# Kernel tuning notes

Measured on AMD Instinct MI355X. Metric: run time of the kernel, lower is better.

The kernel has to match this reference:

```python
import jax, jax.numpy as jnp
import numpy as np

STRIDES = (8, 16, 32, 64, 128)
SCORE_THRESH = 0.05
IOU_THRESH = 0.6
MAX_DET = 1000


def _flat(p):
    # [B,C,H,W] -> [B,H*W,C]
    B, C = p.shape[0], p.shape[1]
    return jnp.transpose(p, (0, 2, 3, 1)).reshape(B, -1, C)


def _coords(h, w, stride):
    # FCOS coords_fmap2orig: center of each stride cell, (x, y) order -> [h*w, 2]
    sx = (jnp.arange(w, dtype=jnp.float32) * stride + stride // 2)
    sy = (jnp.arange(h, dtype=jnp.float32) * stride + stride // 2)
    yy, xx = jnp.meshgrid(sy, sx, indexing='ij')
    return jnp.stack([xx.ravel(), yy.ravel()], axis=-1)


def _nms_keep(boxes, valid, thr):
    # boxes: [M,4] sorted by descending score; valid: [M] bool. Greedy NMS keep mask.
    x1, y1, x2, y2 = boxes[:, 0], boxes[:, 1], boxes[:, 2], boxes[:, 3]
    area = (x2 - x1 + 1.0) * (y2 - y1 + 1.0)
    xx1 = jnp.maximum(x1[:, None], x1[None, :])
    yy1 = jnp.maximum(y1[:, None], y1[None, :])
    xx2 = jnp.minimum(x2[:, None], x2[None, :])
    yy2 = jnp.minimum(y2[:, None], y2[None, :])
    inter = jnp.clip(xx2 - xx1, 0.0) * jnp.clip(yy2 - yy1, 0.0)
    iou = inter / (area[:, None] + area[None, :] - inter)
    M = boxes.shape[0]
    idx = jnp.arange(M)

    def body(i, keep):
        sup = (idx > i) & (iou[i] > thr) & keep[i]
        return keep & (~sup)

    return jax.lax.fori_loop(0, M, body, valid)


def setup_inputs() -> dict:
    key = jax.random.key(0)
    B, C = 16, 80
    sizes = [(128, 128), (64, 64), (32, 32), (16, 16), (8, 8)]
    ks = jax.random.split(key, 15)
    inp = {}
    for i, (h, w) in enumerate(sizes):
        lvl = i + 3
        inp[f'cls_p{lvl}'] = jax.random.normal(ks[3 * i], (B, C, h, w), jnp.float32)
        inp[f'cnt_p{lvl}'] = jax.random.normal(ks[3 * i + 1], (B, 1, h, w), jnp.float32)
        inp[f'reg_p{lvl}'] = jax.random.uniform(ks[3 * i + 2], (B, 4, h, w), jnp.float32) * 100.0
    return inp


def _detect(cls_levels, cnt_levels, reg_levels):
    cls_logits = jnp.concatenate([_flat(p) for p in cls_levels], axis=1)  # [B,N,80]
    cnt_logits = jnp.concatenate([_flat(p) for p in cnt_levels], axis=1)  # [B,N,1]
    reg_preds = jnp.concatenate([_flat(p) for p in reg_levels], axis=1)   # [B,N,4]
    coords = jnp.concatenate(
        [_coords(p.shape[2], p.shape[3], s) for p, s in zip(cls_levels, STRIDES)], axis=0)  # [N,2]

    cls_preds = jax.nn.sigmoid(cls_logits)
    cnt_preds = jax.nn.sigmoid(cnt_logits)[..., 0]                        # [B,N]
    cls_max = jnp.max(cls_preds, axis=-1)                                 # [B,N]
    cls_classes = jnp.argmax(cls_preds, axis=-1) + 1                      # [B,N] 1-based labels
    scores = jnp.sqrt(cls_max * cnt_preds)                                # add_centerness

    boxes = jnp.concatenate(
        [coords[None] - reg_preds[..., :2], coords[None] + reg_preds[..., 2:]], axis=-1)  # [B,N,4]

    M = min(MAX_DET, scores.shape[1])
    topv, topi = jax.lax.top_k(scores, M)                                 # sorted desc
    classes_k = jnp.take_along_axis(cls_classes, topi, axis=1)            # [B,M]
    boxes_k = jnp.take_along_axis(boxes, topi[..., None], axis=1)         # [B,M,4]
    valid = topv >= SCORE_THRESH

    def per_image(b, s, c, v):
        # class-aware NMS via coordinate offset trick
        off = c.astype(b.dtype) * (jnp.max(b) + 1.0)
        keep = _nms_keep(b + off[:, None], v, IOU_THRESH)
        kf = keep.astype(s.dtype)
        return s * kf, c * keep.astype(c.dtype), b * kf[:, None]

    return jax.vmap(per_image)(boxes_k, topv, classes_k, valid)


def reference(cls_p3, cnt_p3, reg_p3, cls_p4, cnt_p4, reg_p4, cls_p5, cnt_p5, reg_p5,
              cls_p6, cnt_p6, reg_p6, cls_p7, cnt_p7, reg_p7):
    cls_levels = [cls_p3, cls_p4, cls_p5, cls_p6, cls_p7]
    cnt_levels = [cnt_p3, cnt_p4, cnt_p5, cnt_p6, cnt_p7]
    reg_levels = [reg_p3, reg_p4, reg_p5, reg_p6, reg_p7]
    return _detect(cls_levels, cnt_levels, reg_levels)
```

## Files before the change

### kernel.cpp

```cpp
#include <hip/hip_runtime.h>
#include <math.h>

#define NB 16
#define NC 80
#define NA 21824
#define NM 1000
#define NHBINS 2048
#define CANDCAP 4096

#define OFF_KEYS     0ul
#define OFF_CLSV     2793472ul
#define OFF_TOPSCORE 4190208ul
#define OFF_TOPCLS   4254208ul
#define OFF_TOPBOX   4318208ul
#define OFF_MAXB     4574208ul
#define OFF_MASK     4574272ul

__device__ __forceinline__ float sigm(float x) { return 1.0f / (1.0f + expf(-x)); }

__global__ __launch_bounds__(256, 6) void k_score(
    const float* __restrict__ cls3, const float* __restrict__ cnt3,
    const float* __restrict__ cls4, const float* __restrict__ cnt4,
    const float* __restrict__ cls5, const float* __restrict__ cnt5,
    const float* __restrict__ cls6, const float* __restrict__ cnt6,
    const float* __restrict__ cls7, const float* __restrict__ cnt7,
    unsigned long long* __restrict__ keys,
    float* __restrict__ clsv)
{
    __shared__ float lm[4 * 64 * 4];
    __shared__ int   lam[4 * 64 * 4];
    __shared__ float cm[256];
    __shared__ int   cam[256];
    const int b = blockIdx.y;
    const int tid = threadIdx.x;
    const int a = tid & 63, s = tid >> 6;
    const int g4 = blockIdx.x * 64 + a;

    if (g4 < (NA >> 2)) {
        const int n = g4 << 2;
        const float* clsP; int off, logW;
        if      (n < 16384) { clsP = cls3; off = 0;     logW = 7; }
        else if (n < 20480) { clsP = cls4; off = 16384; logW = 6; }
        else if (n < 21504) { clsP = cls5; off = 20480; logW = 5; }
        else if (n < 21760) { clsP = cls6; off = 21504; logW = 4; }
        else                { clsP = cls7; off = 21760; logW = 3; }
        const int HW4 = 1 << (2 * logW - 2);
        const int l4 = (n - off) >> 2;
        const float4* cp = (const float4*)clsP + (size_t)b * NC * HW4 + l4;
        const int c0 = s * 20;
        float4 buf[4];
#pragma unroll
        for (int u = 0; u < 4; u++) buf[u] = cp[(size_t)(c0 + u) * HW4];
        float m[4] = { -3.402823466e+38f, -3.402823466e+38f, -3.402823466e+38f, -3.402823466e+38f };
        int am[4] = { c0, c0, c0, c0 };
#pragma unroll
        for (int u = 0; u < 20; u++) {
            float4 vv = buf[u & 3];
            if (u + 4 < 20) buf[u & 3] = cp[(size_t)(c0 + u + 4) * HW4];
            const int c = c0 + u;
            if (vv.x > m[0]) { m[0] = vv.x; am[0] = c; }
            if (vv.y > m[1]) { m[1] = vv.y; am[1] = c; }
            if (vv.z > m[2]) { m[2] = vv.z; am[2] = c; }
            if (vv.w > m[3]) { m[3] = vv.w; am[3] = c; }
        }
#pragma unroll
        for (int k = 0; k < 4; k++) { lm[tid * 4 + k] = m[k]; lam[tid * 4 + k] = am[k]; }
    }
    __syncthreads();
    if (tid < 64 && (blockIdx.x * 64 + tid) < (NA >> 2)) {
        float M[4]; int AM[4];
#pragma unroll
        for (int k = 0; k < 4; k++) { M[k] = lm[tid * 4 + k]; AM[k] = lam[tid * 4 + k]; }
        for (int s2 = 1; s2 < 4; s2++) {
#pragma unroll
            for (int k = 0; k < 4; k++) {
                float vv = lm[(s2 * 64 + tid) * 4 + k];
                if (vv > M[k]) { M[k] = vv; AM[k] = lam[(s2 * 64 + tid) * 4 + k]; }
            }
        }
#pragma unroll
        for (int k = 0; k < 4; k++) { cm[tid * 4 + k] = M[k]; cam[tid * 4 + k] = AM[k]; }
    }
    __syncthreads();
    const int n2 = blockIdx.x * 256 + tid;
    if (n2 < NA) {
        const float* cntP; int off, logW;
        if      (n2 < 16384) { cntP = cnt3; off = 0;     logW = 7; }
        else if (n2 < 20480) { cntP = cnt4; off = 16384; logW = 6; }
        else if (n2 < 21504) { cntP = cnt5; off = 20480; logW = 5; }
        else if (n2 < 21760) { cntP = cnt6; off = 21504; logW = 4; }
        else                 { cntP = cnt7; off = 21760; logW = 3; }
        const int HW = 1 << (2 * logW);
        const int local = n2 - off;
        float cn = cntP[(size_t)b * HW + local];
        float M = cm[tid]; int AM = cam[tid];
        float sc = sqrtf(sigm(M) * sigm(cn));
        unsigned long long key = ((unsigned long long)__float_as_uint(sc) << 32)
                               | (unsigned int)(~(unsigned int)n2);
        keys[(size_t)b * NA + n2] = key;
        clsv[(size_t)b * NA + n2] = (float)(AM + 1);
    }
}

__global__ __launch_bounds__(256) void k_mid(
    const unsigned long long* __restrict__ keys, const float* __restrict__ clsv,
    const float* __restrict__ reg3, const float* __restrict__ reg4, const float* __restrict__ reg5,
    const float* __restrict__ reg6, const float* __restrict__ reg7,
    float* __restrict__ topscore, float* __restrict__ topcls,
    float4* __restrict__ topbox, float* __restrict__ maxb)
{
    __shared__ unsigned int sh_hist[NHBINS];
    __shared__ unsigned int sh_cur[NHBINS];
    __shared__ unsigned int sh_off[NHBINS];
    __shared__ unsigned int sh_subh[NHBINS];
    __shared__ unsigned int sh_subo[NHBINS];
    __shared__ unsigned int sh_subc[NHBINS];
    __shared__ unsigned long long scand[CANDCAP];
    __shared__ unsigned long long scand2[CANDCAP];
    __shared__ int part1[256];
    __shared__ int part2[8];
    __shared__ int sBoundary;
    __shared__ float redmax[256];

    const int b = blockIdx.x;
    const int tid = threadIdx.x;
    const unsigned long long* kb = keys + (size_t)b * NA;
    const ulonglong2* k2 = (const ulonglong2*)kb;

    for (int i = tid; i < NHBINS; i += 256) {
        sh_hist[i] = 0u; sh_cur[i] = 0u; sh_subh[i] = 0u; sh_subc[i] = 0u;
    }
    __syncthreads();

    for (int i = tid; i < NA / 2; i += 256) {
        ulonglong2 v = k2[i];
        atomicAdd(&sh_hist[(unsigned int)(v.x >> 51)], 1u);
        atomicAdd(&sh_hist[(unsigned int)(v.y >> 51)], 1u);
    }
    __syncthreads();

    { int s = 0; for (int i = 0; i < 8; i++) s += (int)sh_hist[tid * 8 + i]; part1[tid] = s; }
    __syncthreads();
    if (tid < 8) { int s2 = 0; for (int t = 0; t < 32; t++) s2 += part1[tid * 32 + t]; part2[tid] = s2; }
    __syncthreads();

    if (tid == 0) {
        int acc = 0, sc;
        for (sc = 7; sc > 0; sc--) { if (acc + part2[sc] >= NM) break; acc += part2[sc]; }
        int t;
        for (t = sc * 32 + 31; t > sc * 32; t--) { if (acc + part1[t] >= NM) break; acc += part1[t]; }
        int bin;
        for (bin = t * 8 + 7; bin > t * 8; bin--) { if (acc + (int)sh_hist[bin] >= NM) break; acc += (int)sh_hist[bin]; }
        sBoundary = bin;
    }
    {
        const int g = tid >> 5;
        int acc = 0;
        for (int q = g + 1; q < 8; q++) acc += part2[q];
        for (int t2 = (g << 5) + 31; t2 > tid; t2--) acc += part1[t2];
        int run = acc;
        for (int k = 7; k >= 0; k--) { sh_off[tid * 8 + k] = (unsigned int)run; run += (int)sh_hist[tid * 8 + k]; }
    }
    __syncthreads();

    const unsigned int boundary = (unsigned int)sBoundary;
    int total = (int)(sh_off[boundary] + sh_hist[boundary]);
    int cnt = (total > CANDCAP) ? CANDCAP : total;
    const int s0 = (int)sh_off[boundary];
    const int Lb = cnt - s0;

    for (int i = tid; i < NA / 2; i += 256) {
        ulonglong2 v = k2[i];
        unsigned int b0 = (unsigned int)(v.x >> 51);
        if (b0 >= boundary) { unsigned int p = sh_off[b0] + atomicAdd(&sh_cur[b0], 1u); if (p < CANDCAP) scand[p] = v.x; }
        unsigned int b1 = (unsigned int)(v.y >> 51);
        if (b1 >= boundary) { unsigned int p = sh_off[b1] + atomicAdd(&sh_cur[b1], 1u); if (p < CANDCAP) scand[p] = v.y; }
    }
    __syncthreads();

    for (int k = tid; k < Lb; k += 256)
        atomicAdd(&sh_subh[(unsigned int)(scand[s0 + k] >> 40) & 2047u], 1u);
    __syncthreads();

    { int s = 0; for (int i = 0; i < 8; i++) s += (int)sh_subh[tid * 8 + i]; part1[tid] = s; }
    __syncthreads();
    if (tid < 8) { int s2 = 0; for (int t = 0; t < 32; t++) s2 += part1[tid * 32 + t]; part2[tid] = s2; }
    __syncthreads();
    {
        const int g = tid >> 5;
        int acc = 0;
        for (int q = g + 1; q < 8; q++) acc += part2[q];
        for (int t2 = (g << 5) + 31; t2 > tid; t2--) acc += part1[t2];
        int run = acc;
        for (int k = 7; k >= 0; k--) { sh_subo[tid * 8 + k] = (unsigned int)run; run += (int)sh_subh[tid * 8 + k]; }
    }
    __syncthreads();

    for (int k = tid; k < Lb; k += 256) {
        unsigned long long v = scand[s0 + k];
        unsigned int sb = (unsigned int)(v >> 40) & 2047u;
        unsigned int p = sh_subo[sb] + atomicAdd(&sh_subc[sb], 1u);
        scand2[p] = v;
    }
    __syncthreads();

    float mymax = -3.402823466e+38f;
    for (int idx = tid; idx < cnt; idx += 256) {
        const unsigned long long key = (idx < s0) ? scand[idx] : scand2[idx - s0];
        const unsigned int bin = (unsigned int)(key >> 51);
        int rank;
        if (bin > boundary) {
            int g0 = (int)sh_off[bin];
            int g1 = g0 + (int)sh_hist[bin];
            rank = g0;
            for (int j = g0; j < g1; j++) rank += (scand[j] > key);
        } else {
            unsigned int sb = (unsigned int)(key >> 40) & 2047u;
            int t0 = (int)sh_subo[sb];
            int t1 = t0 + (int)sh_subh[sb];
            rank = s0 + t0;
            for (int j = t0; j < t1; j++) rank += (scand2[j] > key);
        }
        if (rank < NM) {
            const unsigned int ai = ~(unsigned int)key;
            const float* regP; int lvloff, W, logW, st;
            if      (ai < 16384) { regP = reg3; lvloff = 0;     W = 128; logW = 7; st = 8;   }
            else if (ai < 20480) { regP = reg4; lvloff = 16384; W = 64;  logW = 6; st = 16;  }
            else if (ai < 21504) { regP = reg5; lvloff = 20480; W = 32;  logW = 5; st = 32;  }
            else if (ai < 21760) { regP = reg6; lvloff = 21504; W = 16;  logW = 4; st = 64;  }
            else                 { regP = reg7; lvloff = 21760; W = 8;   logW = 3; st = 128; }
            const int local = (int)ai - lvloff;
            const int HW = 1 << (2 * logW);
            const float* rp = regP + (size_t)b * 4 * HW + local;
            float r0 = rp[0], r1 = rp[HW], r2 = rp[2 * HW], r3 = rp[3 * HW];
            float cv = clsv[(size_t)b * NA + ai];
            const float hs = (float)(st >> 1);
            float cx = (float)((local & (W - 1)) * st) + hs;
            float cy = (float)((local >> logW) * st) + hs;
            float4 bxv = make_float4(cx - r0, cy - r1, cx + r2, cy + r3);
            topscore[b * NM + rank] = __uint_as_float((unsigned int)(key >> 32));
            topcls[b * NM + rank] = cv;
            topbox[b * NM + rank] = bxv;
            mymax = fmaxf(mymax, fmaxf(fmaxf(bxv.x, bxv.y), fmaxf(bxv.z, bxv.w)));
        }
    }
    redmax[tid] = mymax;
    __syncthreads();
    for (int sgap = 128; sgap > 0; sgap >>= 1) {
        if (tid < sgap) redmax[tid] = fmaxf(redmax[tid], redmax[tid + sgap]);
        __syncthreads();
    }
    if (tid == 0) maxb[b] = __fadd_rn(redmax[0], 1.0f);
}

__global__ __launch_bounds__(256) void k_iou(
    const float4* __restrict__ topbox, const float* __restrict__ topcls,
    const float* __restrict__ maxb, unsigned long long* __restrict__ maskArr)
{
    __shared__ float4 sB[NM];
    __shared__ float sA[NM];
    const int b = blockIdx.y;
    const int tid = threadIdx.x;
    const float mp1 = maxb[b];
    for (int r = tid; r < NM; r += 256) {
        float4 f = topbox[b * NM + r];
        float off = __fmul_rn(topcls[b * NM + r], mp1);
        f.x = __fadd_rn(f.x, off); f.y = __fadd_rn(f.y, off);
        f.z = __fadd_rn(f.z, off); f.w = __fadd_rn(f.w, off);
        sB[r] = f;
        sA[r] = __fmul_rn(__fadd_rn(__fsub_rn(f.z, f.x), 1.0f),
                          __fadd_rn(__fsub_rn(f.w, f.y), 1.0f));
    }
    __syncthreads();
    int task = blockIdx.x * 256 + tid;
    if (task >= NM * 16) return;
    int w = task / NM, i = task - w * NM;
    float4 bi = sB[i]; float ai = sA[i];
    unsigned long long bits = 0ULL;
    int j0 = w << 6;
    int jstart = (j0 > i + 1) ? j0 : i + 1;
    int jend = (j0 + 64 < NM) ? j0 + 64 : NM;
    for (int j = jstart; j < jend; j++) {
        float4 bj = sB[j];
        float xx1 = fmaxf(bi.x, bj.x);
        float yy1 = fmaxf(bi.y, bj.y);
        float xx2 = fminf(bi.z, bj.z);
        float yy2 = fminf(bi.w, bj.w);
        float iw = fmaxf(__fsub_rn(xx2, xx1), 0.0f);
        float ih = fmaxf(__fsub_rn(yy2, yy1), 0.0f);
        float inter = __fmul_rn(iw, ih);
        float denom = __fsub_rn(__fadd_rn(ai, sA[j]), inter);
        float iou = inter / denom;
        if (iou > 0.6f) bits |= (1ULL << (j - j0));
    }
    maskArr[((size_t)b * 16 + w) * NM + i] = bits;
}

__global__ __launch_bounds__(256) void k_nms_sweep(
    const unsigned long long* __restrict__ maskArr,
    const float* __restrict__ topscore, const float* __restrict__ topcls,
    const float4* __restrict__ topbox, float* __restrict__ out)
{
    __shared__ unsigned long long smask[16 * NM];
    __shared__ unsigned long long lremv[16];
    const int b = blockIdx.x;
    const int tid = threadIdx.x;
    const int j = tid & 63, q = tid >> 6;
    const unsigned long long* gmask = maskArr + (size_t)b * (16 * NM);

    {
        const ulonglong2* src = (const ulonglong2*)gmask;
        ulonglong2* dst = (ulonglong2*)smask;
        for (int idx = tid; idx < 8 * NM; idx += 256) dst[idx] = src[idx];
    }
    if (tid < 16) lremv[tid] = 0ULL;
    __syncthreads();
    for (int r = tid; r < NM; r += 256) {
        float s = topscore[b * NM + r];
        if (!(s >= 0.05f)) atomicOr(&lremv[r >> 6], 1ULL << (r & 63));
    }

    for (int w = 0; w < 16; w++) {
        __syncthreads();
        const int row = w * 64 + j;
        unsigned long long D = (row < NM) ? smask[w * NM + row] : 0ULL;
        unsigned int dlo = (unsigned int)D, dhi = (unsigned int)(D >> 32);
        unsigned long long sv = lremv[w];
        unsigned int slo = __builtin_amdgcn_readfirstlane((unsigned int)sv);
        unsigned int shi = __builtin_amdgcn_readfirstlane((unsigned int)(sv >> 32));
        unsigned long long s = ((unsigned long long)shi << 32) | slo;
#pragma unroll
        for (int bb = 0; bb < 64; bb++) {
            unsigned int rlo = __builtin_amdgcn_readlane(dlo, bb);
            unsigned int rhi = __builtin_amdgcn_readlane(dhi, bb);
            unsigned long long rowv = ((unsigned long long)rhi << 32) | rlo;
            unsigned long long t = s | rowv;
            s = ((s >> bb) & 1ULL) ? s : t;
        }
        if (tid == 0) lremv[w] = s;
        const unsigned long long kw = ~s;
        if ((kw >> j) & 1ULL) {
            for (int k = w + 1 + q; k < 16; k += 4) {
                unsigned long long v = (row < NM) ? smask[k * NM + row] : 0ULL;
                if (v) atomicOr(&lremv[k], v);
            }
        }
    }
    __syncthreads();

    for (int r = tid; r < NM; r += 256) {
        bool keep = !((lremv[r >> 6] >> (r & 63)) & 1ULL);
        float kf = keep ? 1.0f : 0.0f;
        out[b * NM + r] = topscore[b * NM + r] * kf;
        out[NB * NM + b * NM + r] = topcls[b * NM + r] * kf;
        float4 bx = topbox[b * NM + r];
        ((float4*)(out + 2 * NB * NM))[b * NM + r] = make_float4(bx.x * kf, bx.y * kf, bx.z * kf, bx.w * kf);
    }
}

extern "C" void kernel_launch(void* const* d_in, const int* in_sizes, int n_in,
                              void* d_out, int out_size, void* d_ws, size_t ws_size,
                              hipStream_t stream) {
    const float* cls3 = (const float*)d_in[0];
    const float* cnt3 = (const float*)d_in[1];
    const float* reg3 = (const float*)d_in[2];
    const float* cls4 = (const float*)d_in[3];
    const float* cnt4 = (const float*)d_in[4];
    const float* reg4 = (const float*)d_in[5];
    const float* cls5 = (const float*)d_in[6];
    const float* cnt5 = (const float*)d_in[7];
    const float* reg5 = (const float*)d_in[8];
    const float* cls6 = (const float*)d_in[9];
    const float* cnt6 = (const float*)d_in[10];
    const float* reg6 = (const float*)d_in[11];
    const float* cls7 = (const float*)d_in[12];
    const float* cnt7 = (const float*)d_in[13];
    const float* reg7 = (const float*)d_in[14];

    char* ws = (char*)d_ws;
    unsigned long long* keys   = (unsigned long long*)(ws + OFF_KEYS);
    float*              clsv   = (float*)(ws + OFF_CLSV);
    float*              topsc  = (float*)(ws + OFF_TOPSCORE);
    float*              topcl  = (float*)(ws + OFF_TOPCLS);
    float4*             topbx  = (float4*)(ws + OFF_TOPBOX);
    float*              maxbF  = (float*)(ws + OFF_MAXB);
    unsigned long long* maskA  = (unsigned long long*)(ws + OFF_MASK);

    dim3 g1(86, NB);
    k_score<<<g1, 256, 0, stream>>>(cls3, cnt3, cls4, cnt4, cls5, cnt5,
                                    cls6, cnt6, cls7, cnt7,
                                    keys, clsv);
    k_mid<<<dim3(NB), 256, 0, stream>>>(keys, clsv, reg3, reg4, reg5, reg6, reg7,
                                        topsc, topcl, topbx, maxbF);
    dim3 g4(63, NB);
    k_iou<<<g4, 256, 0, stream>>>(topbx, topcl, maxbF, maskA);
    k_nms_sweep<<<NB, 256, 0, stream>>>(maskA, topsc, topcl, topbx, (float*)d_out);
}
```

Measured before the change: 297.2 us.

## Widen top-k selection block to 1024 threads and rescan keys for boundary bin

The per-image top-k kernel now runs with 1024 threads instead of 256, and its prefix-sum bookkeeping is reshaped to 2 bins per thread and 32 groups. Instead of compacting every candidate at or above the boundary bin into shared memory and then re-reading them to sub-histogram the boundary bin, it builds the boundary sub-histogram during the first scatter pass. A third pass over global keys then places boundary-bin entries directly into their sorted sub-bins. This is meant to cut the serial work per thread in a kernel that uses only 16 blocks. The cost is an extra read of the keys from global memory.

```diff
diff --git a/kernel.cpp b/kernel.cpp
--- a/kernel.cpp
+++ b/kernel.cpp
@@ -7,6 +7,7 @@
 #define NM 1000
 #define NHBINS 2048
 #define CANDCAP 4096
+#define BSZ 1024
 
 #define OFF_KEYS     0ul
 #define OFF_CLSV     2793472ul
@@ -102,7 +103,7 @@
     }
 }
 
-__global__ __launch_bounds__(256) void k_mid(
+__global__ __launch_bounds__(BSZ) void k_mid(
     const unsigned long long* __restrict__ keys, const float* __restrict__ clsv,
     const float* __restrict__ reg3, const float* __restrict__ reg4, const float* __restrict__ reg5,
     const float* __restrict__ reg6, const float* __restrict__ reg7,
@@ -115,109 +116,117 @@
     __shared__ unsigned int sh_subh[NHBINS];
     __shared__ unsigned int sh_subo[NHBINS];
     __shared__ unsigned int sh_subc[NHBINS];
-    __shared__ unsigned long long scand[CANDCAP];
+    __shared__ unsigned long long scand[NM];
     __shared__ unsigned long long scand2[CANDCAP];
-    __shared__ int part1[256];
-    __shared__ int part2[8];
+    __shared__ int part1[BSZ];
+    __shared__ int part2[32];
     __shared__ int sBoundary;
-    __shared__ float redmax[256];
+    __shared__ float redmax[BSZ];
 
     const int b = blockIdx.x;
     const int tid = threadIdx.x;
-    const unsigned long long* kb = keys + (size_t)b * NA;
-    const ulonglong2* k2 = (const ulonglong2*)kb;
-
-    for (int i = tid; i < NHBINS; i += 256) {
+    const ulonglong2* k2 = (const ulonglong2*)(keys + (size_t)b * NA);
+
+    for (int i = tid; i < NHBINS; i += BSZ) {
         sh_hist[i] = 0u; sh_cur[i] = 0u; sh_subh[i] = 0u; sh_subc[i] = 0u;
     }
     __syncthreads();
 
-    for (int i = tid; i < NA / 2; i += 256) {
+    for (int i = tid; i < NA / 2; i += BSZ) {
         ulonglong2 v = k2[i];
         atomicAdd(&sh_hist[(unsigned int)(v.x >> 51)], 1u);
         atomicAdd(&sh_hist[(unsigned int)(v.y >> 51)], 1u);
     }
     __syncthreads();
 
-    { int s = 0; for (int i = 0; i < 8; i++) s += (int)sh_hist[tid * 8 + i]; part1[tid] = s; }
-    __syncthreads();
-    if (tid < 8) { int s2 = 0; for (int t = 0; t < 32; t++) s2 += part1[tid * 32 + t]; part2[tid] = s2; }
+    part1[tid] = (int)sh_hist[2 * tid] + (int)sh_hist[2 * tid + 1];
+    __syncthreads();
+    if (tid < 32) { int s2 = 0; for (int t = 0; t < 32; t++) s2 += part1[tid * 32 + t]; part2[tid] = s2; }
     __syncthreads();
 
     if (tid == 0) {
-        int acc = 0, sc;
-        for (sc = 7; sc > 0; sc--) { if (acc + part2[sc] >= NM) break; acc += part2[sc]; }
+        int acc = 0, g;
+        for (g = 31; g > 0; g--) { if (acc + part2[g] >= NM) break; acc += part2[g]; }
         int t;
-        for (t = sc * 32 + 31; t > sc * 32; t--) { if (acc + part1[t] >= NM) break; acc += part1[t]; }
-        int bin;
-        for (bin = t * 8 + 7; bin > t * 8; bin--) { if (acc + (int)sh_hist[bin] >= NM) break; acc += (int)sh_hist[bin]; }
+        for (t = g * 32 + 31; t > g * 32; t--) { if (acc + part1[t] >= NM) break; acc += part1[t]; }
+        int bin = 2 * t + 1;
+        if (acc + (int)sh_hist[bin] < NM) { acc += (int)sh_hist[bin]; bin = 2 * t; }
         sBoundary = bin;
     }
     {
         const int g = tid >> 5;
         int acc = 0;
-        for (int q = g + 1; q < 8; q++) acc += part2[q];
+        for (int q = g + 1; q < 32; q++) acc += part2[q];
         for (int t2 = (g << 5) + 31; t2 > tid; t2--) acc += part1[t2];
-        int run = acc;
-        for (int k = 7; k >= 0; k--) { sh_off[tid * 8 + k] = (unsigned int)run; run += (int)sh_hist[tid * 8 + k]; }
+        sh_off[2 * tid + 1] = (unsigned int)acc;
+        sh_off[2 * tid]     = (unsigned int)(acc + (int)sh_hist[2 * tid + 1]);
     }
     __syncthreads();
 
     const unsigned int boundary = (unsigned int)sBoundary;
-    int total = (int)(sh_off[boundary] + sh_hist[boundary]);
-    int cnt = (total > CANDCAP) ? CANDCAP : total;
     const int s0 = (int)sh_off[boundary];
-    const int Lb = cnt - s0;
-
-    for (int i = tid; i < NA / 2; i += 256) {
+
+    for (int i = tid; i < NA / 2; i += BSZ) {
         ulonglong2 v = k2[i];
-        unsigned int b0 = (unsigned int)(v.x >> 51);
-        if (b0 >= boundary) { unsigned int p = sh_off[b0] + atomicAdd(&sh_cur[b0], 1u); if (p < CANDCAP) scand[p] = v.x; }
-        unsigned int b1 = (unsigned int)(v.y >> 51);
-        if (b1 >= boundary) { unsigned int p = sh_off[b1] + atomicAdd(&sh_cur[b1], 1u); if (p < CANDCAP) scand[p] = v.y; }
-    }
-    __syncthreads();
-
-    for (int k = tid; k < Lb; k += 256)
-        atomicAdd(&sh_subh[(unsigned int)(scand[s0 + k] >> 40) & 2047u], 1u);
-    __syncthreads();
-
-    { int s = 0; for (int i = 0; i < 8; i++) s += (int)sh_subh[tid * 8 + i]; part1[tid] = s; }
-    __syncthreads();
-    if (tid < 8) { int s2 = 0; for (int t = 0; t < 32; t++) s2 += part1[tid * 32 + t]; part2[tid] = s2; }
+#pragma unroll
+        for (int h = 0; h < 2; h++) {
+            const unsigned long long kk = h ? v.y : v.x;
+            const unsigned int bb = (unsigned int)(kk >> 51);
+            if (bb > boundary) {
+                unsigned int p = sh_off[bb] + atomicAdd(&sh_cur[bb], 1u);
+                if (p < (unsigned int)NM) scand[p] = kk;
+            } else if (bb == boundary) {
+                atomicAdd(&sh_subh[(unsigned int)(kk >> 40) & 2047u], 1u);
+            }
+        }
+    }
+    __syncthreads();
+
+    part1[tid] = (int)sh_subh[2 * tid] + (int)sh_subh[2 * tid + 1];
+    __syncthreads();
+    if (tid < 32) { int s2 = 0; for (int t = 0; t < 32; t++) s2 += part1[tid * 32 + t]; part2[tid] = s2; }
     __syncthreads();
     {
         const int g = tid >> 5;
         int acc = 0;
-        for (int q = g + 1; q < 8; q++) acc += part2[q];
+        for (int q = g + 1; q < 32; q++) acc += part2[q];
         for (int t2 = (g << 5) + 31; t2 > tid; t2--) acc += part1[t2];
-        int run = acc;
-        for (int k = 7; k >= 0; k--) { sh_subo[tid * 8 + k] = (unsigned int)run; run += (int)sh_subh[tid * 8 + k]; }
-    }
-    __syncthreads();
-
-    for (int k = tid; k < Lb; k += 256) {
-        unsigned long long v = scand[s0 + k];
-        unsigned int sb = (unsigned int)(v >> 40) & 2047u;
-        unsigned int p = sh_subo[sb] + atomicAdd(&sh_subc[sb], 1u);
-        scand2[p] = v;
-    }
-    __syncthreads();
-
+        sh_subo[2 * tid + 1] = (unsigned int)acc;
+        sh_subo[2 * tid]     = (unsigned int)(acc + (int)sh_subh[2 * tid + 1]);
+    }
+    __syncthreads();
+
+    for (int i = tid; i < NA / 2; i += BSZ) {
+        ulonglong2 v = k2[i];
+#pragma unroll
+        for (int h = 0; h < 2; h++) {
+            const unsigned long long kk = h ? v.y : v.x;
+            if ((unsigned int)(kk >> 51) == boundary) {
+                unsigned int sb = (unsigned int)(kk >> 40) & 2047u;
+                unsigned int p = sh_subo[sb] + atomicAdd(&sh_subc[sb], 1u);
+                if (p < CANDCAP) scand2[p] = kk;
+            }
+        }
+    }
+    __syncthreads();
+
+    int Lbs = (int)sh_hist[boundary]; if (Lbs > CANDCAP) Lbs = CANDCAP;
+    const int cnt = s0 + Lbs;
     float mymax = -3.402823466e+38f;
-    for (int idx = tid; idx < cnt; idx += 256) {
-        const unsigned long long key = (idx < s0) ? scand[idx] : scand2[idx - s0];
-        const unsigned int bin = (unsigned int)(key >> 51);
-        int rank;
-        if (bin > boundary) {
+    for (int idx = tid; idx < cnt; idx += BSZ) {
+        unsigned long long key; int rank;
+        if (idx < s0) {
+            key = scand[idx];
+            const unsigned int bin = (unsigned int)(key >> 51);
             int g0 = (int)sh_off[bin];
-            int g1 = g0 + (int)sh_hist[bin];
+            int g1 = g0 + (int)sh_hist[bin]; if (g1 > s0) g1 = s0;
             rank = g0;
             for (int j = g0; j < g1; j++) rank += (scand[j] > key);
         } else {
-            unsigned int sb = (unsigned int)(key >> 40) & 2047u;
+            key = scand2[idx - s0];
+            const unsigned int sb = (unsigned int)(key >> 40) & 2047u;
             int t0 = (int)sh_subo[sb];
-            int t1 = t0 + (int)sh_subh[sb];
+            int t1 = t0 + (int)sh_subh[sb]; if (t1 > Lbs) t1 = Lbs;
             rank = s0 + t0;
             for (int j = t0; j < t1; j++) rank += (scand2[j] > key);
         }
@@ -246,7 +255,7 @@
     }
     redmax[tid] = mymax;
     __syncthreads();
-    for (int sgap = 128; sgap > 0; sgap >>= 1) {
+    for (int sgap = BSZ / 2; sgap > 0; sgap >>= 1) {
         if (tid < sgap) redmax[tid] = fmaxf(redmax[tid], redmax[tid + sgap]);
         __syncthreads();
     }
@@ -390,7 +399,7 @@
     k_score<<<g1, 256, 0, stream>>>(cls3, cnt3, cls4, cnt4, cls5, cnt5,
                                     cls6, cnt6, cls7, cnt7,
                                     keys, clsv);
-    k_mid<<<dim3(NB), 256, 0, stream>>>(keys, clsv, reg3, reg4, reg5, reg6, reg7,
+    k_mid<<<dim3(NB), BSZ, 0, stream>>>(keys, clsv, reg3, reg4, reg5, reg6, reg7,
                                         topsc, topcl, topbx, maxbF);
     dim3 g4(63, NB);
     k_iou<<<g4, 256, 0, stream>>>(topbx, topcl, maxbF, maskA);
```

Result: faster. 265.4 us, median of 2 (-10.7%).
